# Kernel optimization log

Measured on AMD Instinct MI355X. Metric: run time of the kernel, lower is better.

The kernel has to match this reference:

```python
import jax, jax.numpy as jnp
import numpy as np

# DCNv3Bottleneck(c1=256, c2=256, shortcut=True, g=4, e=0.5, kernel_size=3)
N, C1, C2, H, W = 8, 256, 256, 56, 56
CMID = 128                      # c_ = int(c2 * e)
G, KS, PAD, DIL, STRIDE = 4, 3, 1, 1, 1
K2 = KS * KS                    # 9 sampling points
EPS = 1e-5


def conv2d(x, w, stride=1, pad=0, groups=1):
    return jax.lax.conv_general_dilated(
        x, w, (stride, stride), [(pad, pad), (pad, pad)],
        feature_group_count=groups,
        dimension_numbers=('NCHW', 'OIHW', 'NCHW'))


def bn(x, g, b, m, v):  # inference BatchNorm2d, NCHW
    inv = jax.lax.rsqrt(v + EPS)
    return x * (g * inv).reshape(1, -1, 1, 1) + (b - m * g * inv).reshape(1, -1, 1, 1)


def layernorm(x, g, b):  # over last (channel) axis
    mu = x.mean(-1, keepdims=True)
    var = x.var(-1, keepdims=True)
    return (x - mu) * jax.lax.rsqrt(var + EPS) * g + b


def bilinear_sample(v, loc):
    """grid_sample(bilinear, zeros padding, align_corners=False).
    v: (N,G,Hp,Wp,gc) values; loc: (N,G,L,K2,2) normalized (x,y) in [-1,1].
    returns (N,G,L,K2,gc)."""
    n, g, hp, wp, gc = v.shape
    x = (loc[..., 0] + 1) * wp / 2 - 0.5
    y = (loc[..., 1] + 1) * hp / 2 - 0.5
    x0 = jnp.floor(x)
    y0 = jnp.floor(y)
    wx1 = x - x0
    wy1 = y - y0
    x0i = x0.astype(jnp.int32)
    y0i = y0.astype(jnp.int32)
    vf = v.reshape(n, g, hp * wp, gc)

    def gather(yi, xi):
        valid = (yi >= 0) & (yi < hp) & (xi >= 0) & (xi < wp)
        idx = jnp.clip(yi, 0, hp - 1) * wp + jnp.clip(xi, 0, wp - 1)
        out = jnp.take_along_axis(vf, idx.reshape(n, g, -1, 1), axis=2)
        return out.reshape(*idx.shape, gc) * valid[..., None]

    return (gather(y0i, x0i) * ((1 - wy1) * (1 - wx1))[..., None]
            + gather(y0i, x0i + 1) * ((1 - wy1) * wx1)[..., None]
            + gather(y0i + 1, x0i) * (wy1 * (1 - wx1))[..., None]
            + gather(y0i + 1, x0i + 1) * (wy1 * wx1)[..., None])


def dcnv3_core(value, offset, mask):
    """InternImage dcnv3_core_pytorch, offset_scale=1.0.
    value: (N,H,W,C) NHWC; offset: (N,H,W,G*K2*2); mask: (N,H,W,G,K2) softmaxed."""
    n, h, w, c = value.shape
    gc = c // G
    v = jnp.pad(value, ((0, 0), (PAD, PAD), (PAD, PAD), (0, 0)))
    hp, wp = h + 2 * PAD, w + 2 * PAD
    hout, wout = h, w  # stride 1, same padding
    # reference points (centers of output locations), normalized by padded dims
    start = DIL * (KS - 1) / 2 + 0.5
    ry = (start + jnp.arange(hout) * STRIDE) / hp
    rx = (start + jnp.arange(wout) * STRIDE) / wp
    ref = jnp.stack(jnp.meshgrid(rx, ry, indexing='xy'), -1)  # (Hout,Wout,2) = (x,y)
    # dilation kernel grid
    base = -((DIL * (KS - 1)) // 2)
    px = (base + jnp.arange(KS) * DIL) / wp
    py = (base + jnp.arange(KS) * DIL) / hp
    gx, gy = jnp.meshgrid(px, py, indexing='ij')
    kgrid = jnp.stack([gx, gy], -1).reshape(K2, 2)
    # sampling locations: shared base grid per group + learned per-group offsets
    base_loc = ref[None, :, :, None, :] + kgrid[None, None, None, :, :]  # (1,H,W,K2,2)
    off = offset.reshape(n, hout, wout, G, K2, 2) / jnp.array([wp, hp], value.dtype)
    samp = base_loc[:, :, :, None, :, :] + off                           # (N,H,W,G,K2,2)
    grid = (2 * samp - 1).reshape(n, hout * wout, G, K2, 2).transpose(0, 2, 1, 3, 4)
    vg = v.reshape(n, hp, wp, G, gc).transpose(0, 3, 1, 2, 4)            # (N,G,Hp,Wp,gc)
    sampled = bilinear_sample(vg, grid)                                  # (N,G,L,K2,gc)
    m = mask.reshape(n, hout * wout, G, K2).transpose(0, 2, 1, 3)        # (N,G,L,K2)
    out = jnp.einsum('nglk,nglkc->nglc', m, sampled)
    return out.transpose(0, 2, 1, 3).reshape(n, hout, wout, c)


def _forward(x, w_cv1, bn1_g, bn1_b, bn1_m, bn1_v,
             w_dw, b_dw, ln_g, ln_b, w_inp, b_inp,
             w_off, b_off, w_msk, b_msk, w_out, b_out,
             bn2_g, bn2_b, bn2_m, bn2_v):
    # cv1: 3x3 conv -> BN -> SiLU
    h = jax.nn.silu(bn(conv2d(x, w_cv1, 1, 1), bn1_g, bn1_b, bn1_m, bn1_v))  # (N,CMID,H,W)
    # offset/mask branch: depthwise 3x3 -> LN (channels_last) -> GELU
    t = conv2d(h, w_dw, 1, (KS - 1) // 2, groups=CMID) + b_dw.reshape(1, -1, 1, 1)
    t = jax.nn.gelu(layernorm(t.transpose(0, 2, 3, 1), ln_g, ln_b), approximate=False)
    xh = h.transpose(0, 2, 3, 1)                       # NHWC
    value = xh @ w_inp + b_inp                         # input_proj
    offset = t @ w_off + b_off                         # (N,H,W,G*K2*2), shared per group
    mask = jax.nn.softmax((t @ w_msk + b_msk).reshape(*t.shape[:3], G, K2), axis=-1)
    o = dcnv3_core(value, offset, mask)
    o = (o @ w_out + b_out).transpose(0, 3, 1, 2)      # output_proj c_ -> c2, back to NCHW
    o = jax.nn.silu(bn(o, bn2_g, bn2_b, bn2_m, bn2_v))
    return x + o                                       # shortcut (c1 == c2)


def setup_inputs() -> dict:
    key = jax.random.key(0)
    ks = jax.random.split(key, 8)
    rn = lambda k, s, sc=0.02: jax.random.normal(k, s, jnp.float32) * sc
    return {
        'x': jax.random.normal(ks[0], (N, C1, H, W), jnp.float32),
        'w_cv1': rn(ks[1], (CMID, C1, 3, 3)),
        'bn1_g': jnp.ones((CMID,), jnp.float32), 'bn1_b': jnp.zeros((CMID,), jnp.float32),
        'bn1_m': jnp.zeros((CMID,), jnp.float32), 'bn1_v': jnp.ones((CMID,), jnp.float32),
        'w_dw': rn(ks[2], (CMID, 1, KS, KS)), 'b_dw': jnp.zeros((CMID,), jnp.float32),
        'ln_g': jnp.ones((CMID,), jnp.float32), 'ln_b': jnp.zeros((CMID,), jnp.float32),
        'w_inp': rn(ks[3], (CMID, CMID)), 'b_inp': jnp.zeros((CMID,), jnp.float32),
        'w_off': rn(ks[4], (CMID, G * K2 * 2), 0.01), 'b_off': jnp.zeros((G * K2 * 2,), jnp.float32),
        'w_msk': rn(ks[5], (CMID, G * K2), 0.01), 'b_msk': jnp.zeros((G * K2,), jnp.float32),
        'w_out': rn(ks[6], (CMID, C2)), 'b_out': jnp.zeros((C2,), jnp.float32),
        'bn2_g': jnp.ones((C2,), jnp.float32), 'bn2_b': jnp.zeros((C2,), jnp.float32),
        'bn2_m': jnp.zeros((C2,), jnp.float32), 'bn2_v': jnp.ones((C2,), jnp.float32),
    }


def reference(x, w_cv1, bn1_g, bn1_b, bn1_m, bn1_v,
              w_dw, b_dw, ln_g, ln_b, w_inp, b_inp,
              w_off, b_off, w_msk, b_msk, w_out, b_out,
              bn2_g, bn2_b, bn2_m, bn2_v):
    return _forward(x, w_cv1, bn1_g, bn1_b, bn1_m, bn1_v,
                    w_dw, b_dw, ln_g, ln_b, w_inp, b_inp,
                    w_off, b_off, w_msk, b_msk, w_out, b_out,
                    bn2_g, bn2_b, bn2_m, bn2_v)
```

## Files before the change

### kernel.cpp

```cpp
#include <hip/hip_runtime.h>
#include <hip/hip_bf16.h>

typedef __hip_bfloat16 bf16;
typedef float f32x4 __attribute__((ext_vector_type(4)));
typedef short s16x8 __attribute__((ext_vector_type(8)));

#define NN 8
#define HH 56
#define WW 56
#define C1 256
#define CM 128
#define C2 256
#define GG 4
#define K2K 9
#define HWSZ (HH*WW)
#define LL (NN*HWSZ)
#define EPSF 1e-5f
#define XP_H 58
#define XP_W 58

__device__ __forceinline__ float b2f(bf16 v){ return __bfloat162float(v); }

__global__ __launch_bounds__(256) void k0pre(
    const float* __restrict__ x, const float* __restrict__ w,
    const float* __restrict__ wout, const float* __restrict__ winp,
    const float* __restrict__ woff, const float* __restrict__ wmsk,
    const float* __restrict__ g2, const float* __restrict__ bb2,
    const float* __restrict__ m2, const float* __restrict__ v2,
    const float* __restrict__ bout, const float* __restrict__ wdw,
    bf16* __restrict__ xp, bf16* __restrict__ Wf, bf16* __restrict__ Wf2,
    bf16* __restrict__ Wf3, bf16* __restrict__ Wf4,
    float* __restrict__ scbi, float* __restrict__ wdwT)
{
    int bidg = blockIdx.x;
    if (bidg < 1856){
        __shared__ float lds[64][57];
        int n = bidg / 232; int rem = bidg % 232;
        int yp = rem >> 2; int ci0 = (rem & 3) << 6;
        int tid = threadIdx.x;
        bool interior = (yp >= 1 && yp <= 56);
        if (interior){
            int y = yp - 1;
            for (int e = tid; e < 64*56; e += 256){
                int ci = e / 56, xx = e - (e/56)*56;
                lds[ci][xx] = x[((size_t)((n*C1 + ci0 + ci)*HH) + y)*WW + xx];
            }
            __syncthreads();
        }
        for (int g = tid; g < 464; g += 256){
            int pxp = g >> 3, cig = (g & 7) << 3;
            s16x8 v;
            if (!interior || pxp == 0 || pxp == 57){
                #pragma unroll
                for (int j=0;j<8;j++) ((bf16*)&v)[j] = __float2bfloat16(0.f);
            } else {
                #pragma unroll
                for (int j=0;j<8;j++) ((bf16*)&v)[j] = __float2bfloat16(lds[cig+j][pxp-1]);
            }
            *(s16x8*)(xp + ((size_t)(n*XP_H + yp)*XP_W + pxp)*C1 + ci0 + cig) = v;
        }
        return;
    }
    if (bidg < 2000){
        int tlin = (bidg-1856)*256 + threadIdx.x;
        int kt  = tlin >> 9;
        int rem = tlin & 511;
        int nt  = rem >> 6;
        int lane = rem & 63;
        int co = nt*16 + (lane & 15);
        int kbase = kt*32 + (lane >> 4)*8;
        bf16* dst = Wf + (size_t)tlin*8;
        #pragma unroll
        for (int j = 0; j < 8; j++){
            int k = kbase + j;
            int tap = k >> 8;
            int ci  = k & 255;
            dst[j] = __float2bfloat16(w[((size_t)co*C1 + ci)*9 + tap]);
        }
        return;
    }
    int t = (bidg-2000)*256 + threadIdx.x;
    if (t < 4096){
        int lane = t & 63; int kc = (t>>6)&3; int mt = t>>8;
        int co = mt*16 + (lane&15); int k0 = kc*32 + (lane>>4)*8;
        bf16* d = Wf2 + (size_t)t*8;
        #pragma unroll
        for (int j=0;j<8;j++) d[j] = __float2bfloat16(wout[(size_t)(k0+j)*C2 + co]);
    } else if (t < 6144){
        int u = t - 4096; int lane = u&63; int kc=(u>>6)&3; int nt=u>>8;
        int co = nt*16+(lane&15); int k0 = kc*32+(lane>>4)*8;
        bf16* d = Wf3 + (size_t)u*8;
        #pragma unroll
        for (int j=0;j<8;j++) d[j] = __float2bfloat16(winp[(size_t)(k0+j)*CM + co]);
    } else if (t < 7936){
        int u = t - 6144; int lane=u&63; int kc=(u>>6)&3; int nt=u>>8;
        int nn2 = nt*16+(lane&15); int k0 = kc*32+(lane>>4)*8;
        bf16* d = Wf4 + (size_t)u*8;
        #pragma unroll
        for (int j=0;j<8;j++){
            int k = k0+j; float v = 0.f;
            if (nn2 < 72) v = woff[(size_t)k*72 + nn2];
            else if (nn2 < 108) v = wmsk[(size_t)k*36 + (nn2-72)];
            d[j] = __float2bfloat16(v);
        }
    } else if (t < 8192){
        int co = t - 7936;
        float sc = g2[co]*rsqrtf(v2[co]+EPSF);
        scbi[co] = sc;
        scbi[256+co] = bb2[co] - m2[co]*sc + bout[co]*sc;
    } else if (t < 8192 + 9*CM){
        int u = t - 8192;
        int tap = u >> 7, c = u & 127;
        wdwT[tap*CM + c] = wdw[c*9 + tap];
    }
}

__device__ __forceinline__ void stageB(const bf16* __restrict__ Wf, int s, bf16* buf, int w, int lane){
    const bf16* g = Wf + ((size_t)s << 12) + (w << 10) + lane*8;
    bf16* l = buf + (w << 10);
    __builtin_amdgcn_global_load_lds((const __attribute__((address_space(1))) void*)g,
                                     (__attribute__((address_space(3))) void*)l, 16, 0, 0);
    __builtin_amdgcn_global_load_lds((const __attribute__((address_space(1))) void*)(g + 512),
                                     (__attribute__((address_space(3))) void*)(l + 512), 16, 0, 0);
}

__device__ __forceinline__ s16x8 loadA1(const bf16* __restrict__ xp, long abase, int s){
    int tap = s >> 3; int dy = tap/3, dx = tap - dy*3;
    int off = ((dy-1)*XP_W + (dx-1))*C1 + ((s&7)<<5);
    return *(const s16x8*)(xp + abase + off);
}

__global__ __launch_bounds__(256) void k1_mfma(
    const bf16* __restrict__ xp, const bf16* __restrict__ Wf,
    const float* __restrict__ bg, const float* __restrict__ bb,
    const float* __restrict__ bm, const float* __restrict__ bv,
    bf16* __restrict__ hb)
{
    __shared__ __align__(16) bf16 Bbuf[2][8192];
    int bid = blockIdx.x;
    int n = bid/98, p0 = (bid%98)*32;
    int tid = threadIdx.x, lane = tid & 63;
    int w  = tid >> 6;
    int wm = w & 1, wn = w >> 1;
    int kpart = lane >> 4;
    int col = lane & 15;
    int pxA = p0 + wm*16 + col;
    {
    }
    int yA = pxA/WW, xxA = pxA - yA*WW;
    long abase = ((long)((n*XP_H + yA + 1)*XP_W) + (xxA+1))*C1 + kpart*8;

    f32x4 acc[4] = {{0,0,0,0},{0,0,0,0},{0,0,0,0},{0,0,0,0}};

    stageB(Wf, 0, &Bbuf[0][0],    w, lane);
    stageB(Wf, 1, &Bbuf[0][4096], w, lane);
    s16x8 A0 = loadA1(xp, abase, 0);
    s16x8 A1 = loadA1(xp, abase, 1);
    __syncthreads();

    for (int ss = 0; ss < 36; ++ss){
        s16x8 An0 = A0, An1 = A1;
        if (ss + 1 < 36){
            stageB(Wf, 2*ss+2, &Bbuf[(ss+1)&1][0],    w, lane);
            stageB(Wf, 2*ss+3, &Bbuf[(ss+1)&1][4096], w, lane);
            An0 = loadA1(xp, abase, 2*ss+2);
            An1 = loadA1(xp, abase, 2*ss+3);
        }
        const bf16* bufp = &Bbuf[ss&1][0] + (wn << 11) + lane*8;
        #pragma unroll
        for (int ct = 0; ct < 4; ++ct){
            s16x8 bfrag = *(const s16x8*)(bufp + (ct << 9));
            acc[ct] = __builtin_amdgcn_mfma_f32_16x16x32_bf16(A0, bfrag, acc[ct], 0, 0, 0);
        }
        #pragma unroll
        for (int ct = 0; ct < 4; ++ct){
            s16x8 bfrag = *(const s16x8*)(bufp + 4096 + (ct << 9));
            acc[ct] = __builtin_amdgcn_mfma_f32_16x16x32_bf16(A1, bfrag, acc[ct], 0, 0, 0);
        }
        __syncthreads();
        A0 = An0; A1 = An1;
    }

    int pxO = p0 + wm*16 + kpart*4;
    #pragma unroll
    for (int ct = 0; ct < 4; ++ct){
        int co = (wn << 6) + (ct << 4) + col;
        float sc = bg[co] * rsqrtf(bv[co] + EPSF);
        float bi = bb[co] - bm[co]*sc;
        #pragma unroll
        for (int r = 0; r < 4; ++r){
            int px = pxO + r;
            float z = acc[ct][r]*sc + bi;
            float sl = z / (1.f + expf(-z));
            hb[((size_t)n*HWSZ + px)*CM + co] = __float2bfloat16(sl);
        }
    }
}

__global__ __launch_bounds__(256) void k3f(
    const bf16* __restrict__ hb,
    const float* __restrict__ wdwT, const float* __restrict__ bdw,
    const float* __restrict__ lng, const float* __restrict__ lnb,
    const bf16* __restrict__ Wf3, const bf16* __restrict__ Wf4,
    const float* __restrict__ binp, const float* __restrict__ boff, const float* __restrict__ bmsk,
    bf16* __restrict__ val, float* __restrict__ om)
{
    __shared__ __align__(16) bf16 Ah[64*136];
    __shared__ __align__(16) bf16 At[64*136];
    int blk = blockIdx.x;
    int n = blk/49; int p0 = (blk%49)*64;
    size_t pixbase = (size_t)n*HWSZ + p0;
    int tid = threadIdx.x;
    for (int e = tid; e < 1024; e += 256){
        int row = e>>4, seg = e&15;
        *(s16x8*)&Ah[row*136 + seg*8] = *(const s16x8*)(hb + (pixbase+row)*CM + seg*8);
    }
    {
        int slot = tid & 15, c0 = slot*8;
        int pbase = (tid >> 4) * 4;
        const bf16* hbase = hb + (size_t)n*HWSZ*CM;
        float4 b0 = *(const float4*)(bdw + c0);
        float4 b1 = *(const float4*)(bdw + c0 + 4);
        float4 g0 = *(const float4*)(lng + c0); float4 g1 = *(const float4*)(lng + c0+4);
        float4 q0 = *(const float4*)(lnb + c0); float4 q1 = *(const float4*)(lnb + c0+4);
        float gv[8]={g0.x,g0.y,g0.z,g0.w,g1.x,g1.y,g1.z,g1.w};
        float qv[8]={q0.x,q0.y,q0.z,q0.w,q1.x,q1.y,q1.z,q1.w};
        #pragma unroll
        for (int i=0;i<4;i++){
            int pxl = p0 + pbase + i;
            int y = pxl/WW, xq = pxl - (pxl/WW)*WW;
            float acc[8] = {b0.x,b0.y,b0.z,b0.w,b1.x,b1.y,b1.z,b1.w};
            #pragma unroll
            for (int tap=0; tap<9; tap++){
                int dy=tap/3, dx=tap%3;
                int yy=y+dy-1, xx=xq+dx-1;
                if ((unsigned)yy < HH && (unsigned)xx < WW){
                    s16x8 v = *(const s16x8*)(hbase + ((size_t)(yy*WW+xx))*CM + c0);
                    float4 w0 = *(const float4*)(wdwT + tap*CM + c0);
                    float4 w1 = *(const float4*)(wdwT + tap*CM + c0 + 4);
                    float wv[8] = {w0.x,w0.y,w0.z,w0.w,w1.x,w1.y,w1.z,w1.w};
                    #pragma unroll
                    for (int j=0;j<8;j++) acc[j] += b2f(((bf16*)&v)[j]) * wv[j];
                }
            }
            float s1=0.f, s2=0.f;
            #pragma unroll
            for (int j=0;j<8;j++){ s1 += acc[j]; s2 += acc[j]*acc[j]; }
            #pragma unroll
            for (int off=1; off<16; off<<=1){
                s1 += __shfl_xor(s1, off);
                s2 += __shfl_xor(s2, off);
            }
            float mean = s1*(1.f/CM);
            float var  = fmaxf(s2*(1.f/CM) - mean*mean, 0.f);
            float inv  = rsqrtf(var + EPSF);
            s16x8 ov;
            #pragma unroll
            for (int j=0;j<8;j++){
                float z = (acc[j]-mean)*inv*gv[j] + qv[j];
                float gl = 0.5f*z*(1.f + erff(z*0.70710678118654752f));
                ((bf16*)&ov)[j] = __float2bfloat16(gl);
            }
            *(s16x8*)&At[(pbase+i)*136 + c0] = ov;
        }
    }
    __syncthreads();
    int lane = tid & 63, w = tid >> 6;
    int col = lane & 15, kq = lane >> 4;
    s16x8 a0[4], a1[4];
    #pragma unroll
    for (int kc=0;kc<4;kc++){
        a0[kc] = *(const s16x8*)&Ah[(w*16+col)*136 + kc*32 + kq*8];
        a1[kc] = *(const s16x8*)&At[(w*16+col)*136 + kc*32 + kq*8];
    }
    int pxo = p0 + w*16 + kq*4;
    #pragma unroll
    for (int nt=0; nt<8; nt++){
        f32x4 acc = {0,0,0,0};
        #pragma unroll
        for (int kc=0;kc<4;kc++){
            s16x8 b = *(const s16x8*)(Wf3 + ((size_t)(nt*4+kc)*64 + lane)*8);
            acc = __builtin_amdgcn_mfma_f32_16x16x32_bf16(a0[kc], b, acc, 0, 0, 0);
        }
        int co = nt*16 + col;
        float bia = binp[co];
        #pragma unroll
        for (int r=0;r<4;r++)
            val[((size_t)n*HWSZ + pxo + r)*CM + co] = __float2bfloat16(acc[r] + bia);
    }
    #pragma unroll
    for (int nt=0; nt<7; nt++){
        f32x4 acc = {0,0,0,0};
        #pragma unroll
        for (int kc=0;kc<4;kc++){
            s16x8 b = *(const s16x8*)(Wf4 + ((size_t)(nt*4+kc)*64 + lane)*8);
            acc = __builtin_amdgcn_mfma_f32_16x16x32_bf16(a1[kc], b, acc, 0, 0, 0);
        }
        int nn2 = nt*16 + col;
        float bia = (nn2<72) ? boff[nn2] : (nn2<108 ? bmsk[nn2-72] : 0.f);
        #pragma unroll
        for (int r=0;r<4;r++)
            om[((size_t)n*HWSZ + pxo + r)*112 + nn2] = acc[r] + bia;
    }
}

__global__ __launch_bounds__(128) void k4a(
    const bf16* __restrict__ valb, const float* __restrict__ om, bf16* __restrict__ o)
{
    __shared__ float omb[8][112];
    __shared__ float mk[8][36];
    int t = threadIdx.x;
    int pix0 = blockIdx.x*8;
    for (int e = t; e < 8*112; e += 128){
        int p = e / 112, q = e - (e/112)*112;
        omb[p][q] = om[(size_t)(pix0+p)*112 + q];
    }
    __syncthreads();
    if (t < 32){
        int p = t >> 2, g = t & 3;
        float mx = omb[p][72+g*9];
        #pragma unroll
        for (int j=1;j<9;j++) mx = fmaxf(mx, omb[p][72+g*9+j]);
        float sum=0.f; float e9[9];
        #pragma unroll
        for (int j=0;j<9;j++){ e9[j] = expf(omb[p][72+g*9+j]-mx); sum += e9[j]; }
        float inv = 1.f/sum;
        #pragma unroll
        for (int j=0;j<9;j++) mk[p][g*9+j] = e9[j]*inv;
    }
    __syncthreads();
    int p = t >> 4, s = t & 15;
    int g = s >> 2;
    int c0 = s*8;
    int pix = pix0 + p;
    int n = pix / HWSZ, rem = pix % HWSZ;
    int y = rem / WW, xq = rem % WW;
    const bf16* vb = valb + (size_t)n*HWSZ*CM;
    float acc[8] = {0,0,0,0,0,0,0,0};
    #pragma unroll
    for (int k=0;k<9;k++){
        float oxv = omb[p][g*18 + k*2];
        float oyv = omb[p][g*18 + k*2 + 1];
        float sx = (float)xq + (float)(k/3) - 1.f + oxv;
        float sy = (float)y  + (float)(k%3) - 1.f + oyv;
        float x0f = floorf(sx), y0f = floorf(sy);
        float fx = sx - x0f, fy = sy - y0f;
        int x0 = (int)x0f, y0 = (int)y0f;
        float mw = mk[p][g*9+k];
        float w00 = (1.f-fy)*(1.f-fx)*mw;
        float w01 = (1.f-fy)*fx*mw;
        float w10 = fy*(1.f-fx)*mw;
        float w11 = fy*fx*mw;
        if ((unsigned)y0 < HH && (unsigned)x0 < WW){
            s16x8 v = *(const s16x8*)(vb + ((size_t)(y0*WW+x0))*CM + c0);
            #pragma unroll
            for (int j=0;j<8;j++) acc[j] += w00*b2f(((bf16*)&v)[j]);
        }
        if ((unsigned)y0 < HH && (unsigned)(x0+1) < WW){
            s16x8 v = *(const s16x8*)(vb + ((size_t)(y0*WW+x0+1))*CM + c0);
            #pragma unroll
            for (int j=0;j<8;j++) acc[j] += w01*b2f(((bf16*)&v)[j]);
        }
        if ((unsigned)(y0+1) < HH && (unsigned)x0 < WW){
            s16x8 v = *(const s16x8*)(vb + ((size_t)((y0+1)*WW+x0))*CM + c0);
            #pragma unroll
            for (int j=0;j<8;j++) acc[j] += w10*b2f(((bf16*)&v)[j]);
        }
        if ((unsigned)(y0+1) < HH && (unsigned)(x0+1) < WW){
            s16x8 v = *(const s16x8*)(vb + ((size_t)((y0+1)*WW+x0+1))*CM + c0);
            #pragma unroll
            for (int j=0;j<8;j++) acc[j] += w11*b2f(((bf16*)&v)[j]);
        }
    }
    s16x8 ov;
    #pragma unroll
    for (int j=0;j<8;j++) ((bf16*)&ov)[j] = __float2bfloat16(acc[j]);
    *(s16x8*)(o + (size_t)pix*CM + c0) = ov;
}

__global__ __launch_bounds__(256) void k4b(
    const bf16* __restrict__ o, const bf16* __restrict__ Wf2, const float* __restrict__ scbi,
    const float* __restrict__ xin, float* __restrict__ out)
{
    __shared__ __align__(16) bf16 Bl[64*136];
    int blk = blockIdx.x;
    int n = blk/49; int p0 = (blk%49)*64;
    int tid = threadIdx.x;
    for (int e = tid; e < 1024; e += 256){
        int row = e>>4, seg = e&15;
        *(s16x8*)&Bl[row*136 + seg*8] = *(const s16x8*)(o + ((size_t)n*HWSZ + p0 + row)*CM + seg*8);
    }
    __syncthreads();
    int lane = tid & 63, w = tid >> 6;
    int col = lane & 15, kq = lane >> 4;
    int co0 = w*64;
    s16x8 af[4][4];
    #pragma unroll
    for (int mt=0;mt<4;mt++)
        #pragma unroll
        for (int kc=0;kc<4;kc++)
            af[mt][kc] = *(const s16x8*)(Wf2 + (((size_t)((co0>>4)+mt)*4 + kc)*64 + lane)*8);
    f32x4 acc[4][4];
    #pragma unroll
    for (int mt=0;mt<4;mt++)
        #pragma unroll
        for (int nt=0;nt<4;nt++)
            acc[mt][nt] = (f32x4){0,0,0,0};
    #pragma unroll
    for (int nt=0;nt<4;nt++){
        s16x8 bfr[4];
        #pragma unroll
        for (int kc=0;kc<4;kc++)
            bfr[kc] = *(const s16x8*)&Bl[(nt*16+col)*136 + kc*32 + kq*8];
        #pragma unroll
        for (int mt=0;mt<4;mt++)
            #pragma unroll
            for (int kc=0;kc<4;kc++)
                acc[mt][nt] = __builtin_amdgcn_mfma_f32_16x16x32_bf16(af[mt][kc], bfr[kc], acc[mt][nt], 0, 0, 0);
    }
    #pragma unroll
    for (int mt=0;mt<4;mt++){
        #pragma unroll
        for (int r=0;r<4;r++){
            int co = co0 + mt*16 + kq*4 + r;
            float sc = scbi[co], bi = scbi[256+co];
            #pragma unroll
            for (int nt=0;nt<4;nt++){
                int px = p0 + nt*16 + col;
                size_t idx = ((size_t)(n*C2 + co))*HWSZ + px;
                float z = acc[mt][nt][r]*sc + bi;
                float sl = z/(1.f+expf(-z));
                out[idx] = sl + xin[idx];
            }
        }
    }
}

extern "C" void kernel_launch(void* const* d_in, const int* in_sizes, int n_in,
                              void* d_out, int out_size, void* d_ws, size_t ws_size,
                              hipStream_t stream)
{
    const float* x    = (const float*)d_in[0];
    const float* wcv1 = (const float*)d_in[1];
    const float* bn1g = (const float*)d_in[2];
    const float* bn1b = (const float*)d_in[3];
    const float* bn1m = (const float*)d_in[4];
    const float* bn1v = (const float*)d_in[5];
    const float* wdw  = (const float*)d_in[6];
    const float* bdw  = (const float*)d_in[7];
    const float* lng  = (const float*)d_in[8];
    const float* lnb  = (const float*)d_in[9];
    const float* winp = (const float*)d_in[10];
    const float* binp = (const float*)d_in[11];
    const float* woff = (const float*)d_in[12];
    const float* boff = (const float*)d_in[13];
    const float* wmsk = (const float*)d_in[14];
    const float* bmsk = (const float*)d_in[15];
    const float* wout = (const float*)d_in[16];
    const float* bout = (const float*)d_in[17];
    const float* bn2g = (const float*)d_in[18];
    const float* bn2b = (const float*)d_in[19];
    const float* bn2m = (const float*)d_in[20];
    const float* bn2v = (const float*)d_in[21];

    unsigned char* base = (unsigned char*)d_ws;
    bf16*  Wf   = (bf16*)(base);
    bf16*  Wf2  = (bf16*)(base + 589824);
    bf16*  Wf3  = (bf16*)(base + 655360);
    bf16*  Wf4  = (bf16*)(base + 688128);
    float* scbi = (float*)(base + 716800);
    float* wdwT = (float*)(base + 718848);
    bf16*  xp   = (bf16*)(base + 723456);
    bf16*  val  = (bf16*)(base + 723456);
    bf16*  hb   = (bf16*)(base + 14502400);
    float* om   = (float*)(base + 20924928);
    bf16*  o    = (bf16*)(base + 32164352);

    hipLaunchKernelGGL(k0pre, dim3(2037), dim3(256), 0, stream,
                       x, wcv1, wout, winp, woff, wmsk, bn2g, bn2b, bn2m, bn2v, bout, wdw,
                       xp, Wf, Wf2, Wf3, Wf4, scbi, wdwT);
    hipLaunchKernelGGL(k1_mfma, dim3(NN*98), dim3(256), 0, stream,
                       xp, Wf, bn1g, bn1b, bn1m, bn1v, hb);
    hipLaunchKernelGGL(k3f, dim3(NN*49), dim3(256), 0, stream,
                       hb, wdwT, bdw, lng, lnb, Wf3, Wf4, binp, boff, bmsk, val, om);
    hipLaunchKernelGGL(k4a, dim3(LL/8), dim3(128), 0, stream, val, om, o);
    hipLaunchKernelGGL(k4b, dim3(NN*49), dim3(256), 0, stream, o, Wf2, scbi, x, (float*)d_out);
}
```

Before: 243.1 us.

## Split fused depthwise-LN-GELU and projection GEMM kernel into two kernels

```diff
diff --git a/kernel.cpp b/kernel.cpp
--- a/kernel.cpp
+++ b/kernel.cpp
@@ -145,8 +145,6 @@
     int kpart = lane >> 4;
     int col = lane & 15;
     int pxA = p0 + wm*16 + col;
-    {
-    }
     int yA = pxA/WW, xxA = pxA - yA*WW;
     long abase = ((long)((n*XP_H + yA + 1)*XP_W) + (xxA+1))*C1 + kpart*8;
 
@@ -197,85 +195,94 @@
     }
 }
 
-__global__ __launch_bounds__(256) void k3f(
-    const bf16* __restrict__ hb,
-    const float* __restrict__ wdwT, const float* __restrict__ bdw,
-    const float* __restrict__ lng, const float* __restrict__ lnb,
+__global__ __launch_bounds__(128) void k2v(
+    const bf16* __restrict__ hb, const float* __restrict__ wdwT, const float* __restrict__ bdw,
+    const float* __restrict__ lng, const float* __restrict__ lnb, bf16* __restrict__ tb)
+{
+    int t = threadIdx.x;
+    int p = t >> 4, s = t & 15;
+    int pix = blockIdx.x*8 + p;
+    int n = pix / HWSZ, rem = pix % HWSZ;
+    int y = rem / WW, xq = rem % WW;
+    int c0 = s*8;
+    const bf16* hbase = hb + (size_t)n*HWSZ*CM;
+    float acc[8];
+    {
+        float4 b0 = *(const float4*)(bdw + c0);
+        float4 b1 = *(const float4*)(bdw + c0 + 4);
+        acc[0]=b0.x; acc[1]=b0.y; acc[2]=b0.z; acc[3]=b0.w;
+        acc[4]=b1.x; acc[5]=b1.y; acc[6]=b1.z; acc[7]=b1.w;
+    }
+    #pragma unroll
+    for (int tap=0; tap<9; tap++){
+        int dy=tap/3, dx=tap%3;
+        int yy=y+dy-1, xx=xq+dx-1;
+        if ((unsigned)yy < HH && (unsigned)xx < WW){
+            s16x8 v = *(const s16x8*)(hbase + ((size_t)(yy*WW+xx))*CM + c0);
+            float4 w0 = *(const float4*)(wdwT + tap*CM + c0);
+            float4 w1 = *(const float4*)(wdwT + tap*CM + c0 + 4);
+            float wv[8] = {w0.x,w0.y,w0.z,w0.w,w1.x,w1.y,w1.z,w1.w};
+            #pragma unroll
+            for (int j=0;j<8;j++)
+                acc[j] += b2f(((bf16*)&v)[j]) * wv[j];
+        }
+    }
+    float s1=0.f, s2=0.f;
+    #pragma unroll
+    for (int j=0;j<8;j++){ s1 += acc[j]; s2 += acc[j]*acc[j]; }
+    #pragma unroll
+    for (int off=1; off<16; off<<=1){
+        s1 += __shfl_xor(s1, off);
+        s2 += __shfl_xor(s2, off);
+    }
+    float mean = s1*(1.f/CM);
+    float var  = fmaxf(s2*(1.f/CM) - mean*mean, 0.f);
+    float inv  = rsqrtf(var + EPSF);
+    float4 g0 = *(const float4*)(lng + c0); float4 g1 = *(const float4*)(lng + c0+4);
+    float4 q0 = *(const float4*)(lnb + c0); float4 q1 = *(const float4*)(lnb + c0+4);
+    float gv[8]={g0.x,g0.y,g0.z,g0.w,g1.x,g1.y,g1.z,g1.w};
+    float qv[8]={q0.x,q0.y,q0.z,q0.w,q1.x,q1.y,q1.z,q1.w};
+    s16x8 ov;
+    #pragma unroll
+    for (int j=0;j<8;j++){
+        float z = (acc[j]-mean)*inv*gv[j] + qv[j];
+        float gl = 0.5f*z*(1.f + erff(z*0.70710678118654752f));
+        ((bf16*)&ov)[j] = __float2bfloat16(gl);
+    }
+    *(s16x8*)(tb + (size_t)pix*CM + c0) = ov;
+}
+
+__global__ __launch_bounds__(256) void k3_gemm(
+    const bf16* __restrict__ hb, const bf16* __restrict__ tb,
     const bf16* __restrict__ Wf3, const bf16* __restrict__ Wf4,
     const float* __restrict__ binp, const float* __restrict__ boff, const float* __restrict__ bmsk,
     bf16* __restrict__ val, float* __restrict__ om)
 {
-    __shared__ __align__(16) bf16 Ah[64*136];
-    __shared__ __align__(16) bf16 At[64*136];
+    __shared__ __align__(16) bf16 Ah[32*136];
+    __shared__ __align__(16) bf16 At[32*136];
     int blk = blockIdx.x;
-    int n = blk/49; int p0 = (blk%49)*64;
+    int n = blk/98; int p0 = (blk%98)*32;
     size_t pixbase = (size_t)n*HWSZ + p0;
     int tid = threadIdx.x;
-    for (int e = tid; e < 1024; e += 256){
+    for (int e = tid; e < 512; e += 256){
         int row = e>>4, seg = e&15;
         *(s16x8*)&Ah[row*136 + seg*8] = *(const s16x8*)(hb + (pixbase+row)*CM + seg*8);
-    }
-    {
-        int slot = tid & 15, c0 = slot*8;
-        int pbase = (tid >> 4) * 4;
-        const bf16* hbase = hb + (size_t)n*HWSZ*CM;
-        float4 b0 = *(const float4*)(bdw + c0);
-        float4 b1 = *(const float4*)(bdw + c0 + 4);
-        float4 g0 = *(const float4*)(lng + c0); float4 g1 = *(const float4*)(lng + c0+4);
-        float4 q0 = *(const float4*)(lnb + c0); float4 q1 = *(const float4*)(lnb + c0+4);
-        float gv[8]={g0.x,g0.y,g0.z,g0.w,g1.x,g1.y,g1.z,g1.w};
-        float qv[8]={q0.x,q0.y,q0.z,q0.w,q1.x,q1.y,q1.z,q1.w};
-        #pragma unroll
-        for (int i=0;i<4;i++){
-            int pxl = p0 + pbase + i;
-            int y = pxl/WW, xq = pxl - (pxl/WW)*WW;
-            float acc[8] = {b0.x,b0.y,b0.z,b0.w,b1.x,b1.y,b1.z,b1.w};
-            #pragma unroll
-            for (int tap=0; tap<9; tap++){
-                int dy=tap/3, dx=tap%3;
-                int yy=y+dy-1, xx=xq+dx-1;
-                if ((unsigned)yy < HH && (unsigned)xx < WW){
-                    s16x8 v = *(const s16x8*)(hbase + ((size_t)(yy*WW+xx))*CM + c0);
-                    float4 w0 = *(const float4*)(wdwT + tap*CM + c0);
-                    float4 w1 = *(const float4*)(wdwT + tap*CM + c0 + 4);
-                    float wv[8] = {w0.x,w0.y,w0.z,w0.w,w1.x,w1.y,w1.z,w1.w};
-                    #pragma unroll
-                    for (int j=0;j<8;j++) acc[j] += b2f(((bf16*)&v)[j]) * wv[j];
-                }
-            }
-            float s1=0.f, s2=0.f;
-            #pragma unroll
-            for (int j=0;j<8;j++){ s1 += acc[j]; s2 += acc[j]*acc[j]; }
-            #pragma unroll
-            for (int off=1; off<16; off<<=1){
-                s1 += __shfl_xor(s1, off);
-                s2 += __shfl_xor(s2, off);
-            }
-            float mean = s1*(1.f/CM);
-            float var  = fmaxf(s2*(1.f/CM) - mean*mean, 0.f);
-            float inv  = rsqrtf(var + EPSF);
-            s16x8 ov;
-            #pragma unroll
-            for (int j=0;j<8;j++){
-                float z = (acc[j]-mean)*inv*gv[j] + qv[j];
-                float gl = 0.5f*z*(1.f + erff(z*0.70710678118654752f));
-                ((bf16*)&ov)[j] = __float2bfloat16(gl);
-            }
-            *(s16x8*)&At[(pbase+i)*136 + c0] = ov;
-        }
+        *(s16x8*)&At[row*136 + seg*8] = *(const s16x8*)(tb + (pixbase+row)*CM + seg*8);
     }
     __syncthreads();
     int lane = tid & 63, w = tid >> 6;
     int col = lane & 15, kq = lane >> 4;
+    int mt = w & 1, wn = w >> 1;
     s16x8 a0[4], a1[4];
     #pragma unroll
     for (int kc=0;kc<4;kc++){
-        a0[kc] = *(const s16x8*)&Ah[(w*16+col)*136 + kc*32 + kq*8];
-        a1[kc] = *(const s16x8*)&At[(w*16+col)*136 + kc*32 + kq*8];
-    }
-    int pxo = p0 + w*16 + kq*4;
-    #pragma unroll
-    for (int nt=0; nt<8; nt++){
+        a0[kc] = *(const s16x8*)&Ah[(mt*16+col)*136 + kc*32 + kq*8];
+        a1[kc] = *(const s16x8*)&At[(mt*16+col)*136 + kc*32 + kq*8];
+    }
+    int pxo = p0 + mt*16 + kq*4;
+    #pragma unroll
+    for (int nti=0; nti<4; nti++){
+        int nt = wn*4 + nti;
         f32x4 acc = {0,0,0,0};
         #pragma unroll
         for (int kc=0;kc<4;kc++){
@@ -289,18 +296,21 @@
             val[((size_t)n*HWSZ + pxo + r)*CM + co] = __float2bfloat16(acc[r] + bia);
     }
     #pragma unroll
-    for (int nt=0; nt<7; nt++){
-        f32x4 acc = {0,0,0,0};
-        #pragma unroll
-        for (int kc=0;kc<4;kc++){
-            s16x8 b = *(const s16x8*)(Wf4 + ((size_t)(nt*4+kc)*64 + lane)*8);
-            acc = __builtin_amdgcn_mfma_f32_16x16x32_bf16(a1[kc], b, acc, 0, 0, 0);
-        }
-        int nn2 = nt*16 + col;
-        float bia = (nn2<72) ? boff[nn2] : (nn2<108 ? bmsk[nn2-72] : 0.f);
-        #pragma unroll
-        for (int r=0;r<4;r++)
-            om[((size_t)n*HWSZ + pxo + r)*112 + nn2] = acc[r] + bia;
+    for (int nti=0; nti<4; nti++){
+        int nt = wn*4 + nti;
+        if (nt < 7){
+            f32x4 acc = {0,0,0,0};
+            #pragma unroll
+            for (int kc=0;kc<4;kc++){
+                s16x8 b = *(const s16x8*)(Wf4 + ((size_t)(nt*4+kc)*64 + lane)*8);
+                acc = __builtin_amdgcn_mfma_f32_16x16x32_bf16(a1[kc], b, acc, 0, 0, 0);
+            }
+            int nn2 = nt*16 + col;
+            float bia = (nn2<72) ? boff[nn2] : (nn2<108 ? bmsk[nn2-72] : 0.f);
+            #pragma unroll
+            for (int r=0;r<4;r++)
+                om[((size_t)n*HWSZ + pxo + r)*112 + nn2] = acc[r] + bia;
+        }
     }
 }
 
@@ -471,7 +481,8 @@
     float* scbi = (float*)(base + 716800);
     float* wdwT = (float*)(base + 718848);
     bf16*  xp   = (bf16*)(base + 723456);
-    bf16*  val  = (bf16*)(base + 723456);
+    bf16*  tb   = (bf16*)(base + 723456);
+    bf16*  val  = (bf16*)(base + 7145984);
     bf16*  hb   = (bf16*)(base + 14502400);
     float* om   = (float*)(base + 20924928);
     bf16*  o    = (bf16*)(base + 32164352);
@@ -481,8 +492,10 @@
                        xp, Wf, Wf2, Wf3, Wf4, scbi, wdwT);
     hipLaunchKernelGGL(k1_mfma, dim3(NN*98), dim3(256), 0, stream,
                        xp, Wf, bn1g, bn1b, bn1m, bn1v, hb);
-    hipLaunchKernelGGL(k3f, dim3(NN*49), dim3(256), 0, stream,
-                       hb, wdwT, bdw, lng, lnb, Wf3, Wf4, binp, boff, bmsk, val, om);
+    hipLaunchKernelGGL(k2v, dim3(LL/8), dim3(128), 0, stream,
+                       hb, wdwT, bdw, lng, lnb, tb);
+    hipLaunchKernelGGL(k3_gemm, dim3(NN*98), dim3(256), 0, stream,
+                       hb, tb, Wf3, Wf4, binp, boff, bmsk, val, om);
     hipLaunchKernelGGL(k4a, dim3(LL/8), dim3(128), 0, stream, val, om, o);
     hipLaunchKernelGGL(k4b, dim3(NN*49), dim3(256), 0, stream, o, Wf2, scbi, x, (float*)d_out);
 }
```

New measurement: 231.3 us. 4.9% less time.
